# Kernel tuning notes

Hardware: AMD Instinct MI355X
Metric: run time of the kernel (lower is better)

## Reference

```python
import jax, jax.numpy as jnp
import numpy as np

N = 4096        # n_nodes; must equal HID due to the model's mean(dim=1)->classifier quirk
IN_DIM = 512
HID = 4096
E = 65536       # N * avg_degree(16)


def _lin(k, out_dim, in_dim):
    return jax.random.normal(k, (out_dim, in_dim), jnp.float32) * 0.02


def setup_inputs() -> dict:
    key = jax.random.key(0)
    ks = jax.random.split(key, 8)
    return {
        "x": jax.random.normal(ks[0], (N, IN_DIM), jnp.float32),
        "edge_index": jax.random.randint(ks[1], (2, E), 0, N, dtype=jnp.int32),
        "W_embed": _lin(ks[2], HID, IN_DIM),
        "b_embed": jnp.zeros((HID,), jnp.float32),
        "W1": _lin(ks[3], HID, HID),
        "b1": jnp.zeros((HID,), jnp.float32),
        "W2": _lin(ks[4], HID, HID),
        "b2": jnp.zeros((HID,), jnp.float32),
        "Wc1": _lin(ks[5], HID // 2, HID),
        "bc1": jnp.zeros((HID // 2,), jnp.float32),
        "Wc2": _lin(ks[6], 1, HID // 2),
        "bc2": jnp.zeros((1,), jnp.float32),
    }


def reference(x, edge_index, W_embed, b_embed, W1, b1, W2, b2, Wc1, bc1, Wc2, bc2):
    row, col = edge_index[0], edge_index[1]
    # embed: Linear(in_dim, hidden)
    h = x @ W_embed.T + b_embed                       # [N, HID]
    # two GNN layers: gather neighbors, scatter-add, linear + relu
    for W, b in ((W1, b1), (W2, b2)):
        aggr = jax.ops.segment_sum(h[col], row, num_segments=h.shape[0])  # [N, HID]
        h = jax.nn.relu(aggr @ W.T + b)
    # faithful to original: mean over feature dim -> [N] (N == HID)
    hm = jnp.mean(h, axis=1)                          # [HID]
    z = jax.nn.relu(hm @ Wc1.T + bc1)                 # [HID//2]
    out = (z @ Wc2.T + bc2).squeeze(-1)               # scalar
    return out
```

## Files before the change

### kernel.cpp

```cpp
#include <hip/hip_runtime.h>
#include <hip/hip_bf16.h>


#define N_NODES 4096
#define IN_DIM_ 512
#define HID_ 4096
#define NEDGE 65536

typedef float f32x4 __attribute__((ext_vector_type(4)));
typedef float f32x2 __attribute__((ext_vector_type(2)));
typedef unsigned short u16x8 __attribute__((ext_vector_type(8)));
typedef int i32x8 __attribute__((ext_vector_type(8)));

#define ACT_SCALE 8.0f
#define W_SCALE 256.0f
#define G_SCALE 8.0f
#define G_STORE_MUL (8.0f / 2048.0f)

__device__ __forceinline__ unsigned short f2bf(float f) {
  unsigned u = __float_as_uint(f);
  return (unsigned short)((u + 0x7fffu + ((u >> 16) & 1u)) >> 16);
}
__device__ __forceinline__ float bf2f(unsigned short h) {
  return __uint_as_float((unsigned)h << 16);
}
__device__ __forceinline__ unsigned char f2fp8(float f) {
  int w = __builtin_amdgcn_cvt_pk_fp8_f32(f, f, 0, false);
  return (unsigned char)(w & 0xff);
}
__device__ __forceinline__ void fp8x4_acc(int w, float* acc) {
  f32x2 lo = __builtin_amdgcn_cvt_pk_f32_fp8(w, false);
  f32x2 hi = __builtin_amdgcn_cvt_pk_f32_fp8(w, true);
  acc[0] += lo[0]; acc[1] += lo[1]; acc[2] += hi[0]; acc[3] += hi[1];
}

#define SL_X  131072L
#define SL_WE 262144L
#define SL_W1 1310720L
#define SL_W2 2359296L
__global__ __launch_bounds__(256) void cvt_all(
    const float* __restrict__ x, const float* __restrict__ We,
    const float* __restrict__ W1, const float* __restrict__ W2,
    unsigned char* __restrict__ xf8, unsigned char* __restrict__ wef8,
    unsigned char* __restrict__ w1f8, unsigned char* __restrict__ w2f8) {
  long S = (long)blockIdx.x * 256 + threadIdx.x;
  const float* src; unsigned char* dst; float sc; long So; int K, ktb;
  if (S < SL_X)       { src = x;  dst = xf8;  sc = ACT_SCALE; So = S;         K = 512;  ktb = 2; }
  else if (S < SL_WE) { src = We; dst = wef8; sc = W_SCALE;   So = S - SL_X;  K = 512;  ktb = 2; }
  else if (S < SL_W1) { src = W1; dst = w1f8; sc = W_SCALE;   So = S - SL_WE; K = 4096; ktb = 5; }
  else                { src = W2; dst = w2f8; sc = W_SCALE;   So = S - SL_W1; K = 4096; ktb = 5; }
  const long region = So >> 7;
  const int rem = (int)(So & 127);
  const int h = (rem >> 6) & 1, q = (rem >> 4) & 3, m = rem & 15;
  const long R16 = region >> ktb;
  const int kt = (int)(region & ((1 << ktb) - 1));
  const long row = R16 * 16 + m;
  const int k0 = kt * 128 + q * 32 + h * 16;
  const float* p = src + row * K + k0;
  const float4 a = *(const float4*)(p);
  const float4 b = *(const float4*)(p + 4);
  const float4 c = *(const float4*)(p + 8);
  const float4 d = *(const float4*)(p + 12);
  int w0 = __builtin_amdgcn_cvt_pk_fp8_f32(a.x * sc, a.y * sc, 0, false);
  w0 = __builtin_amdgcn_cvt_pk_fp8_f32(a.z * sc, a.w * sc, w0, true);
  int w1 = __builtin_amdgcn_cvt_pk_fp8_f32(b.x * sc, b.y * sc, 0, false);
  w1 = __builtin_amdgcn_cvt_pk_fp8_f32(b.z * sc, b.w * sc, w1, true);
  int w2 = __builtin_amdgcn_cvt_pk_fp8_f32(c.x * sc, c.y * sc, 0, false);
  w2 = __builtin_amdgcn_cvt_pk_fp8_f32(c.z * sc, c.w * sc, w2, true);
  int w3 = __builtin_amdgcn_cvt_pk_fp8_f32(d.x * sc, d.y * sc, 0, false);
  w3 = __builtin_amdgcn_cvt_pk_fp8_f32(d.z * sc, d.w * sc, w3, true);
  *(int4*)(dst + So * 16) = make_int4(w0, w1, w2, w3);
}

__global__ __launch_bounds__(256) void zero_i32(int* __restrict__ p, int n) {
  int i = blockIdx.x * 256 + threadIdx.x;
  if (i < n) p[i] = 0;
}

__global__ __launch_bounds__(256) void hist_rows(const int* __restrict__ row,
                                                 int* __restrict__ counts) {
  int e = blockIdx.x * 256 + threadIdx.x;
  if (e < NEDGE) atomicAdd(&counts[row[e]], 1);
}

__global__ __launch_bounds__(1024) void scan4096(const int* __restrict__ counts,
                                                 int* __restrict__ starts) {
  __shared__ int sa[1024], sb[1024];
  const int t = threadIdx.x;
  const int c0 = counts[t * 4], c1 = counts[t * 4 + 1],
            c2 = counts[t * 4 + 2], c3 = counts[t * 4 + 3];
  const int local = c0 + c1 + c2 + c3;
  sa[t] = local;
  __syncthreads();
  int* src = sa; int* dst = sb;
  for (int off = 1; off < 1024; off <<= 1) {
    int v = src[t];
    if (t >= off) v += src[t - off];
    dst[t] = v;
    __syncthreads();
    int* tmp = src; src = dst; dst = tmp;
  }
  const int excl = (t == 0) ? 0 : src[t - 1];
  starts[t * 4]     = excl;
  starts[t * 4 + 1] = excl + c0;
  starts[t * 4 + 2] = excl + c0 + c1;
  starts[t * 4 + 3] = excl + c0 + c1 + c2;
  if (t == 1023) starts[4096] = excl + local;
}

__global__ __launch_bounds__(256) void fill_adj(const int* __restrict__ row,
                                                const int* __restrict__ col,
                                                const int* __restrict__ starts,
                                                int* __restrict__ cursor,
                                                int* __restrict__ adj) {
  int e = blockIdx.x * 256 + threadIdx.x;
  if (e >= NEDGE) return;
  int r = row[e];
  int p = atomicAdd(&cursor[r], 1);
  adj[starts[r] + p] = col[e];
}

#define GLDS(gp, lp)                                                       \
  __builtin_amdgcn_global_load_lds(                                        \
      (const __attribute__((address_space(1))) void*)(gp),                 \
      (__attribute__((address_space(3))) void*)(lp), 16, 0, 0)

__global__ __launch_bounds__(512, 2) void gemm_mx(
    const unsigned char* __restrict__ A, const unsigned char* __restrict__ B,
    unsigned char* __restrict__ C, int N, int K,
    const float* __restrict__ bias, float mul, int permC) {
  __shared__ unsigned char lds[131072];
  const int t = threadIdx.x;
  const int w = blockIdx.x;
  const int xcd = w & 7, j = w >> 3;
  const int bm = ((xcd & 3) * 4 + (j & 3)) * 256;
  const int bn = ((xcd >> 2) * 8 + (j >> 2)) * 256;
  const int wave = t >> 6, lane = t & 63;
  const int wm = (wave >> 2) * 128, wn = (wave & 3) * 64;
  const int m16 = lane & 15, quad = lane >> 4;

  f32x4 acc[8][4] = {};

  const int KT = K >> 7;
  const unsigned char* Ag = A + ((size_t)(bm >> 4) + (t >> 7)) * KT * 2048 + (t & 127) * 16;
  const unsigned char* Bg = B + ((size_t)(bn >> 4) + (t >> 7)) * KT * 2048 + (t & 127) * 16;
  const size_t istep = (size_t)8192 * KT;
  unsigned char* Als = lds;
  unsigned char* Bls = lds + 65536;
  const int sd = t * 16;
  const int lane16 = lane * 16;

#define STAGE_A(i, kb, dst) GLDS(Ag + (kb) + (size_t)(i) * istep, (dst) + (i) * 8192 + sd)
#define STAGE_B(i, kb, dst) GLDS(Bg + (kb) + (size_t)(i) * istep, (dst) + (i) * 8192 + sd)

#define LDFRAG(dst, base, fb)                                              \
  {                                                                        \
    const unsigned char* _p = (base) + (fb) * 2048 + lane16;               \
    const int4 _lo = *(const int4*)(_p);                                   \
    const int4 _hi = *(const int4*)(_p + 1024);                            \
    dst[0] = _lo.x; dst[1] = _lo.y; dst[2] = _lo.z; dst[3] = _lo.w;        \
    dst[4] = _hi.x; dst[5] = _hi.y; dst[6] = _hi.z; dst[7] = _hi.w;        \
  }

#define MFMA(r, c, afr, bfr)                                               \
  acc[r][c] = __builtin_amdgcn_mfma_scale_f32_16x16x128_f8f6f4(            \
      afr, bfr, acc[r][c], 0, 0, 0, 0x7f7f7f7f, 0, 0x7f7f7f7f)

  const int afb = (wave >> 2) * 8;
  const int bfb = (wave & 3) * 4;

  STAGE_A(0, 0, Als); STAGE_A(1, 0, Als); STAGE_A(2, 0, Als); STAGE_A(3, 0, Als);
  STAGE_B(0, 0, Bls); STAGE_B(1, 0, Bls); STAGE_B(2, 0, Bls); STAGE_B(3, 0, Bls);
  asm volatile("s_waitcnt vmcnt(0)" ::: "memory");
  __builtin_amdgcn_s_barrier();

  i32x8 af[4], bf01[2], bf23[2];

  for (int tt = 0; tt < KT; ++tt) {
    unsigned char* Ab = Als + (tt & 1) * 32768;
    unsigned char* Bb = Bls + (tt & 1) * 32768;
    unsigned char* An = Als + ((tt + 1) & 1) * 32768;
    unsigned char* Bn = Bls + ((tt + 1) & 1) * 32768;
    const int kbn = (tt + 1) * 2048;
    const bool more = (tt + 1) < KT;

    LDFRAG(af[0], Ab, afb + 0);
    LDFRAG(af[1], Ab, afb + 1);
    LDFRAG(af[2], Ab, afb + 2);
    LDFRAG(af[3], Ab, afb + 3);
    LDFRAG(bf01[0], Bb, bfb + 0);
    LDFRAG(bf01[1], Bb, bfb + 1);
    LDFRAG(bf23[0], Bb, bfb + 2);
    LDFRAG(bf23[1], Bb, bfb + 3);
    if (more) {
      STAGE_A(0, kbn, An); STAGE_A(1, kbn, An);
      STAGE_A(2, kbn, An); STAGE_A(3, kbn, An);
    }
    __builtin_amdgcn_s_setprio(1);
    MFMA(0, 0, af[0], bf01[0]); MFMA(0, 1, af[0], bf01[1]);
    MFMA(1, 0, af[1], bf01[0]); MFMA(1, 1, af[1], bf01[1]);
    MFMA(2, 0, af[2], bf01[0]); MFMA(2, 1, af[2], bf01[1]);
    MFMA(3, 0, af[3], bf01[0]); MFMA(3, 1, af[3], bf01[1]);
    __builtin_amdgcn_s_setprio(0);
    if (more) {
      STAGE_B(0, kbn, Bn); STAGE_B(1, kbn, Bn);
      STAGE_B(2, kbn, Bn); STAGE_B(3, kbn, Bn);
    }
    __builtin_amdgcn_s_setprio(1);
    MFMA(0, 2, af[0], bf23[0]); MFMA(0, 3, af[0], bf23[1]);
    MFMA(1, 2, af[1], bf23[0]); MFMA(1, 3, af[1], bf23[1]);
    MFMA(2, 2, af[2], bf23[0]); MFMA(2, 3, af[2], bf23[1]);
    MFMA(3, 2, af[3], bf23[0]); MFMA(3, 3, af[3], bf23[1]);
    __builtin_amdgcn_s_setprio(0);
    LDFRAG(af[0], Ab, afb + 4);
    LDFRAG(af[1], Ab, afb + 5);
    LDFRAG(af[2], Ab, afb + 6);
    LDFRAG(af[3], Ab, afb + 7);
    __builtin_amdgcn_s_setprio(1);
    MFMA(4, 0, af[0], bf01[0]); MFMA(4, 1, af[0], bf01[1]);
    MFMA(5, 0, af[1], bf01[0]); MFMA(5, 1, af[1], bf01[1]);
    MFMA(6, 0, af[2], bf01[0]); MFMA(6, 1, af[2], bf01[1]);
    MFMA(7, 0, af[3], bf01[0]); MFMA(7, 1, af[3], bf01[1]);
    __builtin_amdgcn_s_setprio(0);
    __builtin_amdgcn_s_setprio(1);
    MFMA(4, 2, af[0], bf23[0]); MFMA(4, 3, af[0], bf23[1]);
    MFMA(5, 2, af[1], bf23[0]); MFMA(5, 3, af[1], bf23[1]);
    MFMA(6, 2, af[2], bf23[0]); MFMA(6, 3, af[2], bf23[1]);
    MFMA(7, 2, af[3], bf23[0]); MFMA(7, 3, af[3], bf23[1]);
    __builtin_amdgcn_s_setprio(0);
    if (more) {
      asm volatile("s_waitcnt vmcnt(0)" ::: "memory");
      __builtin_amdgcn_sched_barrier(0);
      __builtin_amdgcn_s_barrier();
    }
  }

#undef MFMA
#undef LDFRAG
#undef STAGE_A
#undef STAGE_B

  if (permC) {
    const int KTN = N >> 7;
#pragma unroll
    for (int r = 0; r < 8; ++r) {
#pragma unroll
      for (int c = 0; c < 4; ++c) {
        const int rb = ((bm + wm) >> 4) + r;
        const int colb = bn + wn + c * 16;
        const float bv = bias ? ACT_SCALE * bias[colb + m16] : 0.0f;
        const size_t base = ((size_t)rb * KTN + (colb >> 7)) * 2048
                          + (((colb >> 4) & 1) << 10)
                          + (((colb >> 5) & 3) << 8) + m16;
#pragma unroll
        for (int i = 0; i < 4; ++i) {
          C[base + (quad * 4 + i) * 16] = f2fp8(acc[r][c][i] * mul + bv);
        }
      }
    }
  } else {
#pragma unroll
    for (int r = 0; r < 8; ++r) {
#pragma unroll
      for (int c = 0; c < 4; ++c) {
        const int row0 = bm + wm + r * 16 + quad * 4;
        const int col = bn + wn + c * 16 + m16;
        const float bv = bias ? ACT_SCALE * bias[col] : 0.0f;
#pragma unroll
        for (int i = 0; i < 4; ++i) {
          C[(size_t)(row0 + i) * N + col] = f2fp8(acc[r][c][i] * mul + bv);
        }
      }
    }
  }
}
#undef GLDS

__global__ __launch_bounds__(64) void aggr_f8out(
    const unsigned char* __restrict__ g, const int* __restrict__ starts,
    const int* __restrict__ adj, const float* __restrict__ bias,
    unsigned char* __restrict__ hout) {
  const int node = blockIdx.x >> 3;
  const int f0 = (blockIdx.x & 7) * 512 + threadIdx.x * 8;
  float acc[8] = {0, 0, 0, 0, 0, 0, 0, 0};
  const int s = starts[node], e = starts[node + 1];
  int j = s;
  for (; j + 4 <= e; j += 4) {
    const int c0 = adj[j], c1 = adj[j + 1], c2 = adj[j + 2], c3 = adj[j + 3];
    int2 v0 = *(const int2*)(g + (size_t)c0 * HID_ + f0);
    int2 v1 = *(const int2*)(g + (size_t)c1 * HID_ + f0);
    int2 v2 = *(const int2*)(g + (size_t)c2 * HID_ + f0);
    int2 v3 = *(const int2*)(g + (size_t)c3 * HID_ + f0);
    fp8x4_acc(v0.x, acc);     fp8x4_acc(v0.y, acc + 4);
    fp8x4_acc(v1.x, acc);     fp8x4_acc(v1.y, acc + 4);
    fp8x4_acc(v2.x, acc);     fp8x4_acc(v2.y, acc + 4);
    fp8x4_acc(v3.x, acc);     fp8x4_acc(v3.y, acc + 4);
  }
  for (; j < e; ++j) {
    int2 v = *(const int2*)(g + (size_t)adj[j] * HID_ + f0);
    fp8x4_acc(v.x, acc);      fp8x4_acc(v.y, acc + 4);
  }
  const float4 b0 = *(const float4*)(bias + f0);
  const float4 b1 = *(const float4*)(bias + f0 + 4);
  const float bb[8] = {b0.x, b0.y, b0.z, b0.w, b1.x, b1.y, b1.z, b1.w};
  float v[8];
#pragma unroll
  for (int i = 0; i < 8; ++i)
    v[i] = ACT_SCALE * fmaxf(acc[i] * (1.0f / G_SCALE) + bb[i], 0.0f);
  int w0 = __builtin_amdgcn_cvt_pk_fp8_f32(v[0], v[1], 0, false);
  w0 = __builtin_amdgcn_cvt_pk_fp8_f32(v[2], v[3], w0, true);
  int w1 = __builtin_amdgcn_cvt_pk_fp8_f32(v[4], v[5], 0, false);
  w1 = __builtin_amdgcn_cvt_pk_fp8_f32(v[6], v[7], w1, true);
  const size_t oaddr = ((size_t)(node >> 4) * 32 + (f0 >> 7)) * 2048
                     + (((f0 >> 4) & 1) << 10)
                     + (((f0 >> 5) & 3) << 8) + ((node & 15) << 4) + (f0 & 15);
  *(int2*)(hout + oaddr) = make_int2(w0, w1);
}

__global__ __launch_bounds__(64) void aggr_mean(
    const unsigned char* __restrict__ g, const int* __restrict__ starts,
    const int* __restrict__ adj, const float* __restrict__ bias,
    float* __restrict__ hm) {
  const int node = blockIdx.x >> 3;
  const int f0 = (blockIdx.x & 7) * 512 + threadIdx.x * 8;
  float acc[8] = {0, 0, 0, 0, 0, 0, 0, 0};
  const int s = starts[node], e = starts[node + 1];
  int j = s;
  for (; j + 4 <= e; j += 4) {
    const int c0 = adj[j], c1 = adj[j + 1], c2 = adj[j + 2], c3 = adj[j + 3];
    int2 v0 = *(const int2*)(g + (size_t)c0 * HID_ + f0);
    int2 v1 = *(const int2*)(g + (size_t)c1 * HID_ + f0);
    int2 v2 = *(const int2*)(g + (size_t)c2 * HID_ + f0);
    int2 v3 = *(const int2*)(g + (size_t)c3 * HID_ + f0);
    fp8x4_acc(v0.x, acc);     fp8x4_acc(v0.y, acc + 4);
    fp8x4_acc(v1.x, acc);     fp8x4_acc(v1.y, acc + 4);
    fp8x4_acc(v2.x, acc);     fp8x4_acc(v2.y, acc + 4);
    fp8x4_acc(v3.x, acc);     fp8x4_acc(v3.y, acc + 4);
  }
  for (; j < e; ++j) {
    int2 v = *(const int2*)(g + (size_t)adj[j] * HID_ + f0);
    fp8x4_acc(v.x, acc);      fp8x4_acc(v.y, acc + 4);
  }
  const float4 b0 = *(const float4*)(bias + f0);
  const float4 b1 = *(const float4*)(bias + f0 + 4);
  const float bb[8] = {b0.x, b0.y, b0.z, b0.w, b1.x, b1.y, b1.z, b1.w};
  float local = 0.f;
#pragma unroll
  for (int i = 0; i < 8; ++i)
    local += fmaxf(acc[i] * (1.0f / G_SCALE) + bb[i], 0.0f);
  for (int off = 32; off > 0; off >>= 1) local += __shfl_down(local, off);
  if (threadIdx.x == 0)
    atomicAdd(&hm[node], local * (1.0f / (float)HID_));
}

__global__ __launch_bounds__(256) void clf1(const float* __restrict__ Wc1,
                                            const float* __restrict__ bc1,
                                            const float* __restrict__ hm,
                                            float* __restrict__ z) {
  const int wave = threadIdx.x >> 6, lane = threadIdx.x & 63;
  const int j = blockIdx.x * 4 + wave;
  const float* w = Wc1 + (size_t)j * HID_;
  float s = 0.f;
  for (int i = lane; i < HID_; i += 64) s += w[i] * hm[i];
  for (int off = 32; off > 0; off >>= 1) s += __shfl_down(s, off);
  if (lane == 0) z[j] = fmaxf(s + bc1[j], 0.0f);
}

__global__ __launch_bounds__(256) void clf2(const float* __restrict__ Wc2,
                                            const float* __restrict__ bc2,
                                            const float* __restrict__ z,
                                            float* __restrict__ out) {
  const int t = threadIdx.x;
  float s = 0.f;
  for (int i = t; i < HID_ / 2; i += 256) s += z[i] * Wc2[i];
  for (int off = 32; off > 0; off >>= 1) s += __shfl_down(s, off);
  __shared__ float ws[4];
  if ((t & 63) == 0) ws[t >> 6] = s;
  __syncthreads();
  if (t == 0) out[0] = ws[0] + ws[1] + ws[2] + ws[3] + bc2[0];
}

extern "C" void kernel_launch(void* const* d_in, const int* in_sizes, int n_in,
                              void* d_out, int out_size, void* d_ws, size_t ws_size,
                              hipStream_t stream) {
  (void)in_sizes; (void)n_in; (void)out_size; (void)ws_size;
  const float* x       = (const float*)d_in[0];
  const int*   edge    = (const int*)d_in[1];
  const int*   row     = edge;
  const int*   col     = edge + NEDGE;
  const float* W_embed = (const float*)d_in[2];
  const float* b_embed = (const float*)d_in[3];
  const float* W1      = (const float*)d_in[4];
  const float* b1      = (const float*)d_in[5];
  const float* W2      = (const float*)d_in[6];
  const float* b2      = (const float*)d_in[7];
  const float* Wc1     = (const float*)d_in[8];
  const float* bc1     = (const float*)d_in[9];
  const float* Wc2     = (const float*)d_in[10];
  const float* bc2     = (const float*)d_in[11];
  float* out = (float*)d_out;

  char* ws = (char*)d_ws;
  size_t off = 0;
  auto alloc = [&](size_t bytes) {
    char* p = ws + off;
    off += (bytes + 255) & ~(size_t)255;
    return p;
  };
  unsigned char*  xf8  = (unsigned char*)alloc((size_t)N_NODES * IN_DIM_);
  unsigned char*  wef8 = (unsigned char*)alloc((size_t)HID_ * IN_DIM_);
  unsigned char*  w1f8 = (unsigned char*)alloc((size_t)HID_ * HID_);
  unsigned char*  w2f8 = (unsigned char*)alloc((size_t)HID_ * HID_);
  unsigned char*  h0f8 = (unsigned char*)alloc((size_t)N_NODES * HID_);
  unsigned char*  h1f8 = (unsigned char*)alloc((size_t)N_NODES * HID_);
  unsigned char*  g    = (unsigned char*)alloc((size_t)N_NODES * HID_);
  int*   counts = (int*)alloc(N_NODES * 4);
  int*   cursor = (int*)alloc(N_NODES * 4);
  float* hm     = (float*)alloc(N_NODES * 4);
  int*   starts = (int*)alloc((N_NODES + 1) * 4);
  int*   adj    = (int*)alloc(NEDGE * 4);
  float* z      = (float*)alloc((HID_ / 2) * 4);

  zero_i32<<<48, 256, 0, stream>>>(counts, 3 * N_NODES);
  hist_rows<<<NEDGE / 256, 256, 0, stream>>>(row, counts);
  scan4096<<<1, 1024, 0, stream>>>(counts, starts);
  fill_adj<<<NEDGE / 256, 256, 0, stream>>>(row, col, starts, cursor, adj);

  cvt_all<<<(int)(SL_W2 / 256), 256, 0, stream>>>(x, W_embed, W1, W2,
                                                  xf8, wef8, w1f8, w2f8);

  gemm_mx<<<256, 512, 0, stream>>>(xf8, wef8, h0f8, HID_, IN_DIM_,
                                   b_embed, G_STORE_MUL, 1);
  gemm_mx<<<256, 512, 0, stream>>>(h0f8, w1f8, g, HID_, HID_,
                                   nullptr, G_STORE_MUL, 0);
  aggr_f8out<<<N_NODES * 8, 64, 0, stream>>>(g, starts, adj, b1, h1f8);
  gemm_mx<<<256, 512, 0, stream>>>(h1f8, w2f8, g, HID_, HID_,
                                   nullptr, G_STORE_MUL, 0);
  aggr_mean<<<N_NODES * 8, 64, 0, stream>>>(g, starts, adj, b2, hm);
  clf1<<<(HID_ / 2) / 4, 256, 0, stream>>>(Wc1, bc1, hm, z);
  clf2<<<1, 256, 0, stream>>>(Wc2, bc2, z, out);
}
```

Baseline: 433.5 us.

## Load B fragments directly from global memory instead of staging through LDS

The FP8 MFMA GEMM stops double-buffering the B tile in shared memory. Each wave now loads its B fragments straight from global memory into registers every K-step, which halves LDS use to 64KB. This removes the LDS writes and reads for B and may allow more blocks per CU. In exchange, B is no longer shared across the two wave rows, so global and L2 traffic for B doubles. The direct loads are also not prefetched, so their latency sits exposed right before the MFMAs.

```diff
diff --git a/kernel.cpp b/kernel.cpp
--- a/kernel.cpp
+++ b/kernel.cpp
@@ -129,7 +129,7 @@
     const unsigned char* __restrict__ A, const unsigned char* __restrict__ B,
     unsigned char* __restrict__ C, int N, int K,
     const float* __restrict__ bias, float mul, int permC) {
-  __shared__ unsigned char lds[131072];
+  __shared__ unsigned char lds[65536];
   const int t = threadIdx.x;
   const int w = blockIdx.x;
   const int xcd = w & 7, j = w >> 3;
@@ -142,16 +142,18 @@
   f32x4 acc[8][4] = {};
 
   const int KT = K >> 7;
-  const unsigned char* Ag = A + ((size_t)(bm >> 4) + (t >> 7)) * KT * 2048 + (t & 127) * 16;
-  const unsigned char* Bg = B + ((size_t)(bn >> 4) + (t >> 7)) * KT * 2048 + (t & 127) * 16;
-  const size_t istep = (size_t)8192 * KT;
+  const size_t fstep = (size_t)KT * 2048;
+  const unsigned char* Ag = A + ((size_t)(bm >> 4) + (t >> 7)) * fstep + (t & 127) * 16;
+  const size_t istep = 4 * fstep;
   unsigned char* Als = lds;
-  unsigned char* Bls = lds + 65536;
   const int sd = t * 16;
   const int lane16 = lane * 16;
 
+  const int afb = (wave >> 2) * 8;
+  const int bfb = (wave & 3) * 4;
+  const unsigned char* Bg2 = B + ((size_t)(bn >> 4) + bfb) * fstep + lane16;
+
 #define STAGE_A(i, kb, dst) GLDS(Ag + (kb) + (size_t)(i) * istep, (dst) + (i) * 8192 + sd)
-#define STAGE_B(i, kb, dst) GLDS(Bg + (kb) + (size_t)(i) * istep, (dst) + (i) * 8192 + sd)
 
 #define LDFRAG(dst, base, fb)                                              \
   {                                                                        \
@@ -162,15 +164,19 @@
     dst[4] = _hi.x; dst[5] = _hi.y; dst[6] = _hi.z; dst[7] = _hi.w;        \
   }
 
+#define LOADB(dst, p)                                                      \
+  {                                                                        \
+    const int4 _lo = *(const int4*)(p);                                    \
+    const int4 _hi = *(const int4*)((p) + 1024);                           \
+    dst[0] = _lo.x; dst[1] = _lo.y; dst[2] = _lo.z; dst[3] = _lo.w;        \
+    dst[4] = _hi.x; dst[5] = _hi.y; dst[6] = _hi.z; dst[7] = _hi.w;        \
+  }
+
 #define MFMA(r, c, afr, bfr)                                               \
   acc[r][c] = __builtin_amdgcn_mfma_scale_f32_16x16x128_f8f6f4(            \
       afr, bfr, acc[r][c], 0, 0, 0, 0x7f7f7f7f, 0, 0x7f7f7f7f)
 
-  const int afb = (wave >> 2) * 8;
-  const int bfb = (wave & 3) * 4;
-
   STAGE_A(0, 0, Als); STAGE_A(1, 0, Als); STAGE_A(2, 0, Als); STAGE_A(3, 0, Als);
-  STAGE_B(0, 0, Bls); STAGE_B(1, 0, Bls); STAGE_B(2, 0, Bls); STAGE_B(3, 0, Bls);
   asm volatile("s_waitcnt vmcnt(0)" ::: "memory");
   __builtin_amdgcn_s_barrier();
 
@@ -178,20 +184,19 @@
 
   for (int tt = 0; tt < KT; ++tt) {
     unsigned char* Ab = Als + (tt & 1) * 32768;
-    unsigned char* Bb = Bls + (tt & 1) * 32768;
     unsigned char* An = Als + ((tt + 1) & 1) * 32768;
-    unsigned char* Bn = Bls + ((tt + 1) & 1) * 32768;
     const int kbn = (tt + 1) * 2048;
     const bool more = (tt + 1) < KT;
 
+    const unsigned char* bp = Bg2 + (size_t)tt * 2048;
+    LOADB(bf01[0], bp);
+    LOADB(bf01[1], bp + fstep);
+    LOADB(bf23[0], bp + 2 * fstep);
+    LOADB(bf23[1], bp + 3 * fstep);
     LDFRAG(af[0], Ab, afb + 0);
     LDFRAG(af[1], Ab, afb + 1);
     LDFRAG(af[2], Ab, afb + 2);
     LDFRAG(af[3], Ab, afb + 3);
-    LDFRAG(bf01[0], Bb, bfb + 0);
-    LDFRAG(bf01[1], Bb, bfb + 1);
-    LDFRAG(bf23[0], Bb, bfb + 2);
-    LDFRAG(bf23[1], Bb, bfb + 3);
     if (more) {
       STAGE_A(0, kbn, An); STAGE_A(1, kbn, An);
       STAGE_A(2, kbn, An); STAGE_A(3, kbn, An);
@@ -202,10 +207,6 @@
     MFMA(2, 0, af[2], bf01[0]); MFMA(2, 1, af[2], bf01[1]);
     MFMA(3, 0, af[3], bf01[0]); MFMA(3, 1, af[3], bf01[1]);
     __builtin_amdgcn_s_setprio(0);
-    if (more) {
-      STAGE_B(0, kbn, Bn); STAGE_B(1, kbn, Bn);
-      STAGE_B(2, kbn, Bn); STAGE_B(3, kbn, Bn);
-    }
     __builtin_amdgcn_s_setprio(1);
     MFMA(0, 2, af[0], bf23[0]); MFMA(0, 3, af[0], bf23[1]);
     MFMA(1, 2, af[1], bf23[0]); MFMA(1, 3, af[1], bf23[1]);
@@ -236,9 +237,9 @@
   }
 
 #undef MFMA
+#undef LOADB
 #undef LDFRAG
 #undef STAGE_A
-#undef STAGE_B
 
   if (permC) {
     const int KTN = N >> 7;
```

New measurement: 435.6 us. About the same (+0.5%).
